# Kernel optimization log

Measured on AMD Instinct MI355X. Metric: run time of the kernel, lower is better.

## Reference

```python
import jax, jax.numpy as jnp
import numpy as np

H = 256        # hidden_dim == num_features
C = 10         # num_classes
N = 100000     # nodes
E = 1600000    # edges
BN_EPS = 1e-5
NEG_SLOPE = 0.1


def _bn(h, gamma, beta):
    # training-mode BatchNorm1d over node dim, biased variance (torch semantics)
    mu = jnp.mean(h, axis=0)
    var = jnp.mean(jnp.square(h - mu), axis=0)
    return (h - mu) * jax.lax.rsqrt(var + BN_EPS) * gamma + beta


def setup_inputs() -> dict:
    key = jax.random.key(0)
    ks = jax.random.split(key, 12)
    s = 1.0 / np.sqrt(H)
    x = jax.random.normal(ks[0], (N, H), dtype=jnp.float32)
    edge_index = jax.random.randint(ks[1], (2, E), 0, N, dtype=jnp.int64)
    return {
        "x": x,
        "edge_index": edge_index,
        # GIN MLP: lin1 -> bn -> relu -> lin2
        "W1": jax.random.uniform(ks[2], (H, H), jnp.float32, -s, s),
        "b1": jnp.zeros((H,), jnp.float32),
        "g_mlp": jnp.ones((H,), jnp.float32),
        "be_mlp": jnp.zeros((H,), jnp.float32),
        "W2": jax.random.uniform(ks[3], (H, H), jnp.float32, -s, s),
        "b2": jnp.zeros((H,), jnp.float32),
        # bn4
        "g4": jnp.ones((H,), jnp.float32),
        "be4": jnp.zeros((H,), jnp.float32),
        # head
        "Wl1": jax.random.uniform(ks[4], (H, H // 2), jnp.float32, -s, s),
        "bl1": jnp.zeros((H // 2,), jnp.float32),
        "Wl3": jax.random.uniform(ks[5], (H // 2, C), jnp.float32, -s, s),
        "bl3": jnp.zeros((C,), jnp.float32),
    }


def reference(x, edge_index, W1, b1, g_mlp, be_mlp, W2, b2, g4, be4, Wl1, bl1, Wl3, bl3):
    lrelu = lambda h: jax.nn.leaky_relu(h, NEG_SLOPE)
    src, dst = edge_index[0], edge_index[1]
    # GINConv: sum-aggregate neighbor messages (source_to_target), eps=0
    agg = jax.ops.segment_sum(x[src], dst, num_segments=x.shape[0])  # [N,H]
    h = agg + x  # (1+eps)*x + sum
    # PyG MLP([H,H,H]): lin -> batch_norm -> relu -> lin (plain last)
    h = jax.nn.relu(_bn(h @ W1 + b1, g_mlp, be_mlp)) @ W2 + b2
    x1 = lrelu(h)                     # relu(conv1(...), 0.1); dropout p=0
    h = lrelu(x1)                     # relu(x1, 0.1)
    h = lrelu(_bn(h, g4, be4))        # relu(bn4(x), 0.1); dropout p=0
    h = x + 0.01 * h                  # residual with original features
    h = lrelu(h @ Wl1 + bl1)
    return h @ Wl3 + bl3              # [N, C]
```

## Files before the change

### kernel.cpp

```cpp
#include <hip/hip_runtime.h>

constexpr int NN = 100000;
constexpr int NE = 1600000;
constexpr int HD = 256;
constexpr int NBUCK = 782;
constexpr int CGRID = 98;

typedef __attribute__((ext_vector_type(4))) float  f32x4;
typedef __attribute__((ext_vector_type(2))) float  f32x2;
typedef __attribute__((ext_vector_type(8))) short  bf16x8;

#if defined(__has_builtin)
#if __has_builtin(__builtin_amdgcn_cvt_pk_f32_fp8) && __has_builtin(__builtin_amdgcn_cvt_pk_fp8_f32)
#define HAVE_FP8_CVT 1
#endif
#endif
#ifndef HAVE_FP8_CVT
#define HAVE_FP8_CVT 0
#endif

__device__ __forceinline__ float bf2f(unsigned short u) {
  union { unsigned int i; float f; } c;
  c.i = ((unsigned int)u) << 16;
  return c.f;
}
__device__ __forceinline__ short f2bf(float f) {
  union { float f; unsigned int i; } c; c.f = f;
  unsigned int i = c.i + 0x7fffu + ((c.i >> 16) & 1u);
  return (short)(i >> 16);
}

__device__ __forceinline__ void gload16(const void* g, void* l) {
  __builtin_amdgcn_global_load_lds(
      (const __attribute__((address_space(1))) unsigned int*)g,
      (__attribute__((address_space(3))) unsigned int*)l, 16, 0, 0);
}

__global__ void k_detect(const int* __restrict__ ew, int* __restrict__ flag) {
  __shared__ int bad;
  if (threadIdx.x == 0) bad = 0;
  __syncthreads();
  int nz = 0;
  for (int i = threadIdx.x; i < 2048; i += 256) nz |= ew[2 * i + 1];
  if (nz) atomicOr(&bad, 1);
  __syncthreads();
  if (threadIdx.x == 0) *flag = (bad == 0) ? 1 : 0;
}

__global__ void k_cvtW(const float* __restrict__ W1, const float* __restrict__ W2,
                       const float* __restrict__ Wl1, const float* __restrict__ Wl3,
                       short* __restrict__ W1T, short* __restrict__ W2T,
                       short* __restrict__ Wl1T, short* __restrict__ Wl3T) {
  int b = blockIdx.x, t = threadIdx.x;
  if (b < 256)       W1T[b * 256 + t]        = f2bf(W1[t * 256 + b]);
  else if (b < 512){ int n = b - 256; W2T[n * 256 + t]  = f2bf(W2[t * 256 + n]); }
  else if (b < 640){ int n = b - 512; Wl1T[n * 256 + t] = f2bf(Wl1[t * 128 + n]); }
  else {
    if (t < 128) {
#pragma unroll
      for (int c = 0; c < 16; ++c)
        Wl3T[c * 128 + t] = (c < 10) ? f2bf(Wl3[t * 10 + c]) : (short)0;
    }
  }
}

#if HAVE_FP8_CVT
__global__ void k_cvtX(const float* __restrict__ x, void* __restrict__ xq) {
  int c = blockIdx.x * 256 + threadIdx.x;
  float4 a = ((const float4*)x)[2 * (size_t)c];
  float4 b = ((const float4*)x)[2 * (size_t)c + 1];
  int p0 = 0, p1 = 0;
  p0 = __builtin_amdgcn_cvt_pk_fp8_f32(a.x, a.y, p0, false);
  p0 = __builtin_amdgcn_cvt_pk_fp8_f32(a.z, a.w, p0, true);
  p1 = __builtin_amdgcn_cvt_pk_fp8_f32(b.x, b.y, p1, false);
  p1 = __builtin_amdgcn_cvt_pk_fp8_f32(b.z, b.w, p1, true);
  ((int2*)xq)[c] = make_int2(p0, p1);
}
#else
__global__ void k_cvtX(const float* __restrict__ x, void* __restrict__ xq) {
  int c = blockIdx.x * 256 + threadIdx.x;
  float4 a = ((const float4*)x)[2 * (size_t)c];
  float4 b = ((const float4*)x)[2 * (size_t)c + 1];
  bf16x8 o;
  o[0] = f2bf(a.x); o[1] = f2bf(a.y); o[2] = f2bf(a.z); o[3] = f2bf(a.w);
  o[4] = f2bf(b.x); o[5] = f2bf(b.y); o[6] = f2bf(b.z); o[7] = f2bf(b.w);
  ((bf16x8*)xq)[c] = o;
}
#endif

__global__ __launch_bounds__(1024) void k_count(const int* __restrict__ ew,
                                                const int* __restrict__ flag,
                                                int* __restrict__ cntmat) {
  __shared__ int lcnt[NBUCK];
  int m64 = *flag;
  int t = threadIdx.x;
  for (int i = t; i < NBUCK; i += 1024) lcnt[i] = 0;
  __syncthreads();
  int base = blockIdx.x * 16384;
#pragma unroll
  for (int u = 0; u < 16; u++) {
    int e = base + u * 1024 + t;
    if (e < NE) {
      int d = m64 ? ew[2 * (NE + e)] : ew[NE + e];
      atomicAdd(&lcnt[d >> 7], 1);
    }
  }
  __syncthreads();
  for (int i = t; i < NBUCK; i += 1024) cntmat[blockIdx.x * NBUCK + i] = lcnt[i];
}

__global__ __launch_bounds__(1024) void k_colscan(int* __restrict__ cntmat,
                                                  int* __restrict__ bases,
                                                  int* __restrict__ off_) {
  __shared__ int tot[1024];
  int t = threadIdx.x;
  int sum = 0;
  if (t < NBUCK) {
    for (int g = 0; g < CGRID; g++) sum += cntmat[g * NBUCK + t];
    tot[t] = sum;
  }
  __syncthreads();
  int v = (t < NBUCK) ? sum : 0;
  for (int o = 1; o < 1024; o <<= 1) {
    int u = (t >= o && t < NBUCK) ? tot[t - o] : 0;
    __syncthreads();
    if (t < NBUCK) tot[t] += u;
    __syncthreads();
  }
  if (t < NBUCK) {
    int b = tot[t] - v;
    bases[t] = b;
    int run = b;
    for (int g = 0; g < CGRID; g++) {
      int c = cntmat[g * NBUCK + t];
      cntmat[g * NBUCK + t] = run;
      run += c;
    }
  }
  if (t == NBUCK) bases[NBUCK] = NE;
  if (t == NBUCK + 1) off_[NN] = NE;
}

__global__ __launch_bounds__(1024) void k_scatter(const int* __restrict__ ew,
                                                  const int* __restrict__ flag,
                                                  const int* __restrict__ cntmat,
                                                  int* __restrict__ pairs) {
  __shared__ int lcur[NBUCK];
  int m64 = *flag;
  int t = threadIdx.x;
  for (int i = t; i < NBUCK; i += 1024) lcur[i] = cntmat[blockIdx.x * NBUCK + i];
  __syncthreads();
  int base = blockIdx.x * 16384;
#pragma unroll
  for (int u = 0; u < 16; u++) {
    int e = base + u * 1024 + t;
    if (e < NE) {
      int d = m64 ? ew[2 * (NE + e)] : ew[NE + e];
      int s = m64 ? ew[2 * e] : ew[e];
      int slot = atomicAdd(&lcur[d >> 7], 1);
      pairs[slot] = s | ((d & 127) << 17);
    }
  }
}

__global__ __launch_bounds__(256) void k_bsort(const int* __restrict__ pairs,
                                               const int* __restrict__ bases,
                                               int* __restrict__ off_,
                                               int* __restrict__ csr) {
  __shared__ int lcnt[128], lofs[128], lcur[128];
  int b = blockIdx.x, t = threadIdx.x;
  int s0 = bases[b], s1 = bases[b + 1];
  if (t < 128) lcnt[t] = 0;
  __syncthreads();
  for (int j = s0 + t; j < s1; j += 256) atomicAdd(&lcnt[(pairs[j] >> 17) & 127], 1);
  __syncthreads();
  int v = (t < 128) ? lcnt[t] : 0;
  if (t < 128) lofs[t] = v;
  __syncthreads();
  for (int o = 1; o < 128; o <<= 1) {
    int u = (t >= o && t < 128) ? lofs[t - o] : 0;
    __syncthreads();
    if (t < 128) lofs[t] += u;
    __syncthreads();
  }
  if (t < 128) {
    int ex = lofs[t] - v;
    lcur[t] = ex;
    int node = b * 128 + t;
    if (node < NN) off_[node] = s0 + ex;
  }
  __syncthreads();
  for (int j = s0 + t; j < s1; j += 256) {
    int p = pairs[j];
    int slot = atomicAdd(&lcur[(p >> 17) & 127], 1);
    csr[s0 + slot] = p & 0x1FFFF;
  }
}

#if HAVE_FP8_CVT
__global__ __launch_bounds__(256) void k_agg2(const void* __restrict__ xq,
                                              const int* __restrict__ off_,
                                              const int* __restrict__ csr,
                                              short* __restrict__ h0) {
  int node = blockIdx.x * 4 + (threadIdx.x >> 6);
  int lane = threadIdx.x & 63;
  const unsigned char* xb = (const unsigned char*)xq;
  size_t boff = (size_t)lane * 4;
  int s0 = off_[node], s1 = off_[node + 1];
  int sw = *(const int*)(xb + (size_t)node * 256 + boff);
  f32x2 slo = __builtin_amdgcn_cvt_pk_f32_fp8(sw, false);
  f32x2 shi = __builtin_amdgcn_cvt_pk_f32_fp8(sw, true);
  float a0 = slo[0], a1 = slo[1], a2 = shi[0], a3 = shi[1];
  int j = s0;
  while (j + 8 <= s1) {
    int idx[8];
#pragma unroll
    for (int u = 0; u < 8; u++) idx[u] = csr[j + u];
    int w[8];
#pragma unroll
    for (int u = 0; u < 8; u++) w[u] = *(const int*)(xb + (size_t)idx[u] * 256 + boff);
#pragma unroll
    for (int u = 0; u < 8; u++) {
      f32x2 lo = __builtin_amdgcn_cvt_pk_f32_fp8(w[u], false);
      f32x2 hi = __builtin_amdgcn_cvt_pk_f32_fp8(w[u], true);
      a0 += lo[0]; a1 += lo[1]; a2 += hi[0]; a3 += hi[1];
    }
    j += 8;
  }
  if (j + 4 <= s1) {
    int idx[4];
#pragma unroll
    for (int u = 0; u < 4; u++) idx[u] = csr[j + u];
    int w[4];
#pragma unroll
    for (int u = 0; u < 4; u++) w[u] = *(const int*)(xb + (size_t)idx[u] * 256 + boff);
#pragma unroll
    for (int u = 0; u < 4; u++) {
      f32x2 lo = __builtin_amdgcn_cvt_pk_f32_fp8(w[u], false);
      f32x2 hi = __builtin_amdgcn_cvt_pk_f32_fp8(w[u], true);
      a0 += lo[0]; a1 += lo[1]; a2 += hi[0]; a3 += hi[1];
    }
    j += 4;
  }
  for (; j < s1; j++) {
    int s = csr[j];
    int w = *(const int*)(xb + (size_t)s * 256 + boff);
    f32x2 lo = __builtin_amdgcn_cvt_pk_f32_fp8(w, false);
    f32x2 hi = __builtin_amdgcn_cvt_pk_f32_fp8(w, true);
    a0 += lo[0]; a1 += lo[1]; a2 += hi[0]; a3 += hi[1];
  }
  ushort4 o;
  o.x = (ushort)f2bf(a0); o.y = (ushort)f2bf(a1);
  o.z = (ushort)f2bf(a2); o.w = (ushort)f2bf(a3);
  *(ushort4*)((ushort*)h0 + (size_t)node * 256 + (size_t)lane * 4) = o;
}
#else
__global__ __launch_bounds__(256) void k_agg2(const void* __restrict__ xq,
                                              const int* __restrict__ off_,
                                              const int* __restrict__ csr,
                                              short* __restrict__ h0) {
  int node = blockIdx.x * 4 + (threadIdx.x >> 6);
  int lane = threadIdx.x & 63;
  const ushort* xu = (const ushort*)xq;
  size_t coff = (size_t)lane * 4;
  int s0 = off_[node], s1 = off_[node + 1];
  ushort4 sv = *(const ushort4*)(xu + (size_t)node * 256 + coff);
  float a0 = bf2f(sv.x), a1 = bf2f(sv.y), a2 = bf2f(sv.z), a3 = bf2f(sv.w);
  int j = s0;
  while (j + 8 <= s1) {
    int idx[8];
#pragma unroll
    for (int u = 0; u < 8; u++) idx[u] = csr[j + u];
    ushort4 v[8];
#pragma unroll
    for (int u = 0; u < 8; u++) v[u] = *(const ushort4*)(xu + (size_t)idx[u] * 256 + coff);
#pragma unroll
    for (int u = 0; u < 8; u++) {
      a0 += bf2f(v[u].x); a1 += bf2f(v[u].y);
      a2 += bf2f(v[u].z); a3 += bf2f(v[u].w);
    }
    j += 8;
  }
  for (; j < s1; j++) {
    int s = csr[j];
    ushort4 v = *(const ushort4*)(xu + (size_t)s * 256 + coff);
    a0 += bf2f(v.x); a1 += bf2f(v.y); a2 += bf2f(v.z); a3 += bf2f(v.w);
  }
  ushort4 o;
  o.x = (ushort)f2bf(a0); o.y = (ushort)f2bf(a1);
  o.z = (ushort)f2bf(a2); o.w = (ushort)f2bf(a3);
  *(ushort4*)((ushort*)h0 + (size_t)node * 256 + coff) = o;
}
#endif

template <int ACT, int TIN, int STATS>
__global__ __launch_bounds__(256, 2) void k_gemm(const short* __restrict__ A,
                                              const short* __restrict__ BT,
                                              const float* __restrict__ bias,
                                              short* __restrict__ C, int M,
                                              const float* __restrict__ tsc,
                                              const float* __restrict__ tsh,
                                              float* __restrict__ gsum,
                                              float* __restrict__ gssq) {
  __shared__ char smem[65536];
  __shared__ float lsc[256], lsh[256];
  __shared__ float lsum[128], lssq[128];
  int tid = threadIdx.x;
  int lane = tid & 63, w = tid >> 6;
  if (TIN) { lsc[tid] = tsc[tid]; lsh[tid] = tsh[tid]; }
  if (STATS && tid < 128) { lsum[tid] = 0.f; lssq[tid] = 0.f; }
  int bm = blockIdx.x >> 1, bn = blockIdx.x & 1;
  int bm0 = bm * 128, bn0 = bn * 128;
  int wm = w >> 1, wn = w & 1;
  int lr = lane & 15, lg = lane >> 4;
  f32x4 acc[4][4] = {};
  __syncthreads();

  bf16x8 stg[4];

#pragma unroll 1
  for (int it = 0; it < 4; ++it) {
    int b = it & 1;
    if (it == 0) {
      if (TIN) {
#pragma unroll
        for (int i = 0; i < 4; ++i) {
          int p = tid + 256 * i, row = p >> 3, s = (p & 7) ^ (row & 7);
          int grow = bm0 + row; if (grow > M - 1) grow = M - 1;
          stg[i] = *(const bf16x8*)(A + (size_t)grow * 256 + s * 8);
        }
      } else {
#pragma unroll
        for (int q = 0; q < 4; ++q) {
          int wc = w * 4 + q;
          int p = wc * 64 + lane, row = p >> 3, s = (p & 7) ^ (row & 7);
          int grow = bm0 + row; if (grow > M - 1) grow = M - 1;
          gload16(A + (size_t)grow * 256 + s * 8, smem + wc * 1024);
        }
      }
#pragma unroll
      for (int q = 0; q < 4; ++q) {
        int wc = w * 4 + q;
        int p = wc * 64 + lane, row = p >> 3, s = (p & 7) ^ (row & 7);
        gload16(BT + (size_t)(bn0 + row) * 256 + s * 8, smem + 16384 + wc * 1024);
      }
      if (TIN) {
#pragma unroll
        for (int i = 0; i < 4; ++i) {
          int p = tid + 256 * i, row = p >> 3, s = (p & 7) ^ (row & 7);
          int k0 = s * 8;
          float4 sc0 = *(const float4*)&lsc[k0], sc1 = *(const float4*)&lsc[k0 + 4];
          float4 sh0 = *(const float4*)&lsh[k0], sh1 = *(const float4*)&lsh[k0 + 4];
          bf16x8 v = stg[i], o;
          o[0] = f2bf(fmaxf(bf2f((unsigned short)v[0]) * sc0.x + sh0.x, 0.f));
          o[1] = f2bf(fmaxf(bf2f((unsigned short)v[1]) * sc0.y + sh0.y, 0.f));
          o[2] = f2bf(fmaxf(bf2f((unsigned short)v[2]) * sc0.z + sh0.z, 0.f));
          o[3] = f2bf(fmaxf(bf2f((unsigned short)v[3]) * sc0.w + sh0.w, 0.f));
          o[4] = f2bf(fmaxf(bf2f((unsigned short)v[4]) * sc1.x + sh1.x, 0.f));
          o[5] = f2bf(fmaxf(bf2f((unsigned short)v[5]) * sc1.y + sh1.y, 0.f));
          o[6] = f2bf(fmaxf(bf2f((unsigned short)v[6]) * sc1.z + sh1.z, 0.f));
          o[7] = f2bf(fmaxf(bf2f((unsigned short)v[7]) * sc1.w + sh1.w, 0.f));
          *(bf16x8*)(smem + p * 16) = o;
        }
      }
      __syncthreads();
    }
    int ktn = (it + 1) * 64;
    if (it < 3) {
      char* nb = smem + (b ^ 1) * 32768;
      if (TIN) {
#pragma unroll
        for (int i = 0; i < 4; ++i) {
          int p = tid + 256 * i, row = p >> 3, s = (p & 7) ^ (row & 7);
          int grow = bm0 + row; if (grow > M - 1) grow = M - 1;
          stg[i] = *(const bf16x8*)(A + (size_t)grow * 256 + ktn + s * 8);
        }
      } else {
#pragma unroll
        for (int q = 0; q < 4; ++q) {
          int wc = w * 4 + q;
          int p = wc * 64 + lane, row = p >> 3, s = (p & 7) ^ (row & 7);
          int grow = bm0 + row; if (grow > M - 1) grow = M - 1;
          gload16(A + (size_t)grow * 256 + ktn + s * 8, nb + wc * 1024);
        }
      }
#pragma unroll
      for (int q = 0; q < 4; ++q) {
        int wc = w * 4 + q;
        int p = wc * 64 + lane, row = p >> 3, s = (p & 7) ^ (row & 7);
        gload16(BT + (size_t)(bn0 + row) * 256 + ktn + s * 8, nb + 16384 + wc * 1024);
      }
    }
    const char* sa = smem + b * 32768;
    const char* sb = sa + 16384;
#pragma unroll
    for (int ks = 0; ks < 2; ++ks) {
      bf16x8 af[4], bfr[4];
#pragma unroll
      for (int mi = 0; mi < 4; ++mi) {
        int row = wm * 64 + mi * 16 + lr;
        int q = (lg + 4 * ks) ^ (row & 7);
        af[mi] = *(const bf16x8*)(sa + row * 128 + q * 16);
      }
#pragma unroll
      for (int ni = 0; ni < 4; ++ni) {
        int row = wn * 64 + ni * 16 + lr;
        int q = (lg + 4 * ks) ^ (row & 7);
        bfr[ni] = *(const bf16x8*)(sb + row * 128 + q * 16);
      }
#pragma unroll
      for (int mi = 0; mi < 4; ++mi)
#pragma unroll
        for (int ni = 0; ni < 4; ++ni)
          acc[mi][ni] = __builtin_amdgcn_mfma_f32_16x16x32_bf16(af[mi], bfr[ni], acc[mi][ni], 0, 0, 0);
    }
    if (TIN && it < 3) {
      char* nb = smem + (b ^ 1) * 32768;
#pragma unroll
      for (int i = 0; i < 4; ++i) {
        int p = tid + 256 * i, row = p >> 3, s = (p & 7) ^ (row & 7);
        int k0 = ktn + s * 8;
        float4 sc0 = *(const float4*)&lsc[k0], sc1 = *(const float4*)&lsc[k0 + 4];
        float4 sh0 = *(const float4*)&lsh[k0], sh1 = *(const float4*)&lsh[k0 + 4];
        bf16x8 v = stg[i], o;
        o[0] = f2bf(fmaxf(bf2f((unsigned short)v[0]) * sc0.x + sh0.x, 0.f));
        o[1] = f2bf(fmaxf(bf2f((unsigned short)v[1]) * sc0.y + sh0.y, 0.f));
        o[2] = f2bf(fmaxf(bf2f((unsigned short)v[2]) * sc0.z + sh0.z, 0.f));
        o[3] = f2bf(fmaxf(bf2f((unsigned short)v[3]) * sc0.w + sh0.w, 0.f));
        o[4] = f2bf(fmaxf(bf2f((unsigned short)v[4]) * sc1.x + sh1.x, 0.f));
        o[5] = f2bf(fmaxf(bf2f((unsigned short)v[5]) * sc1.y + sh1.y, 0.f));
        o[6] = f2bf(fmaxf(bf2f((unsigned short)v[6]) * sc1.z + sh1.z, 0.f));
        o[7] = f2bf(fmaxf(bf2f((unsigned short)v[7]) * sc1.w + sh1.w, 0.f));
        *(bf16x8*)(nb + p * 16) = o;
      }
    }
    __syncthreads();
  }

  short* zs = (short*)smem;
#pragma unroll
  for (int ni = 0; ni < 4; ++ni) {
    int col = wn * 64 + ni * 16 + lr;
    float bv = bias[bn0 + col];
    float ps = 0.f, pq = 0.f;
#pragma unroll
    for (int mi = 0; mi < 4; ++mi) {
#pragma unroll
      for (int r = 0; r < 4; ++r) {
        int row = wm * 64 + mi * 16 + lg * 4 + r;
        float tv = acc[mi][ni][r] + bv;
        if (ACT == 1) tv = tv > 0.f ? tv : 0.01f * tv;
        if (STATS && (bm0 + row) < M) { ps += tv; pq += tv * tv; }
        zs[row * 136 + col] = f2bf(tv);
      }
    }
    if (STATS) {
      ps += __shfl_xor(ps, 16); pq += __shfl_xor(pq, 16);
      ps += __shfl_xor(ps, 32); pq += __shfl_xor(pq, 32);
      if (lane < 16) {
        atomicAdd(&lsum[wn * 64 + ni * 16 + lane], ps);
        atomicAdd(&lssq[wn * 64 + ni * 16 + lane], pq);
      }
    }
  }
  __syncthreads();
  {
    int row = tid >> 1;
    int grow = bm0 + row;
    if (grow < M) {
#pragma unroll
      for (int i = 0; i < 8; ++i) {
        int cs = (tid & 1) * 8 + i;
        bf16x8 v = *(const bf16x8*)((const char*)zs + row * 272 + cs * 16);
        *(bf16x8*)(C + (size_t)grow * 256 + bn0 + cs * 8) = v;
      }
    }
  }
  if (STATS) {
    if (tid < 128) {
      atomicAdd(&gsum[bn0 + tid], lsum[tid]);
      atomicAdd(&gssq[bn0 + tid], lssq[tid]);
    }
  }
}

__global__ void k_bnprep(const float* __restrict__ sum, const float* __restrict__ ssq,
                         const float* __restrict__ g, const float* __restrict__ be,
                         float* __restrict__ scale, float* __restrict__ shift, int M) {
  int c = threadIdx.x;
  float mu = sum[c] / (float)M;
  float var = ssq[c] / (float)M - mu * mu;
  float rs = rsqrtf(var + 1e-5f);
  float sc = g[c] * rs;
  scale[c] = sc;
  shift[c] = be[c] - mu * sc;
}

__global__ __launch_bounds__(256, 2) void k_head(const short* __restrict__ V,
                                                 const float* __restrict__ x,
                                                 const short* __restrict__ BT,
                                                 const float* __restrict__ bl1,
                                                 const short* __restrict__ wl3t,
                                                 const float* __restrict__ bl3,
                                                 const float* __restrict__ tsc,
                                                 const float* __restrict__ tsh,
                                                 float* __restrict__ out, int M) {
  __shared__ char smem[65536];
  __shared__ float lsc[256], lsh[256];
  __shared__ short wl3s[2048];
  int tid = threadIdx.x;
  int lane = tid & 63, w = tid >> 6;
  lsc[tid] = tsc[tid]; lsh[tid] = tsh[tid];
  {
    int p = w * 64 + lane;
    gload16(wl3t + (size_t)p * 8, (char*)wl3s + w * 1024);
  }
  int bm0 = blockIdx.x * 128;
  int wm = w >> 1, wn = w & 1;
  int lr = lane & 15, lg = lane >> 4;
  f32x4 acc[4][4] = {};
  __syncthreads();

  bf16x8 stgv[4];
  float stgx[4][8];

#pragma unroll 1
  for (int it = 0; it < 4; ++it) {
    int b = it & 1;
    if (it == 0) {
#pragma unroll
      for (int i = 0; i < 4; ++i) {
        int p = tid + 256 * i, row = p >> 3, s = (p & 7) ^ (row & 7);
        int grow = bm0 + row; if (grow > M - 1) grow = M - 1;
        size_t base = (size_t)grow * 256 + s * 8;
        stgv[i] = *(const bf16x8*)(V + base);
        *(float4*)&stgx[i][0] = *(const float4*)(x + base);
        *(float4*)&stgx[i][4] = *(const float4*)(x + base + 4);
      }
#pragma unroll
      for (int q = 0; q < 4; ++q) {
        int wc = w * 4 + q;
        int p = wc * 64 + lane, row = p >> 3, s = (p & 7) ^ (row & 7);
        gload16(BT + (size_t)row * 256 + s * 8, smem + 16384 + wc * 1024);
      }
#pragma unroll
      for (int i = 0; i < 4; ++i) {
        int p = tid + 256 * i, row = p >> 3, s = (p & 7) ^ (row & 7);
        int k0 = s * 8;
        bf16x8 v = stgv[i], o;
#pragma unroll
        for (int jj = 0; jj < 8; ++jj) {
          float f = bf2f((unsigned short)v[jj]) * lsc[k0 + jj] + lsh[k0 + jj];
          f = f > 0.f ? f : 0.1f * f;
          o[jj] = f2bf(stgx[i][jj] + 0.01f * f);
        }
        *(bf16x8*)(smem + p * 16) = o;
      }
      __syncthreads();
    }
    int ktn = (it + 1) * 64;
    if (it < 3) {
      char* nb = smem + (b ^ 1) * 32768;
#pragma unroll
      for (int i = 0; i < 4; ++i) {
        int p = tid + 256 * i, row = p >> 3, s = (p & 7) ^ (row & 7);
        int grow = bm0 + row; if (grow > M - 1) grow = M - 1;
        size_t base = (size_t)grow * 256 + ktn + s * 8;
        stgv[i] = *(const bf16x8*)(V + base);
        *(float4*)&stgx[i][0] = *(const float4*)(x + base);
        *(float4*)&stgx[i][4] = *(const float4*)(x + base + 4);
      }
#pragma unroll
      for (int q = 0; q < 4; ++q) {
        int wc = w * 4 + q;
        int p = wc * 64 + lane, row = p >> 3, s = (p & 7) ^ (row & 7);
        gload16(BT + (size_t)row * 256 + ktn + s * 8, nb + 16384 + wc * 1024);
      }
    }
    const char* sa = smem + b * 32768;
    const char* sb = sa + 16384;
#pragma unroll
    for (int ks = 0; ks < 2; ++ks) {
      bf16x8 af[4], bfr[4];
#pragma unroll
      for (int mi = 0; mi < 4; ++mi) {
        int row = wm * 64 + mi * 16 + lr;
        int q = (lg + 4 * ks) ^ (row & 7);
        af[mi] = *(const bf16x8*)(sa + row * 128 + q * 16);
      }
#pragma unroll
      for (int ni = 0; ni < 4; ++ni) {
        int row = wn * 64 + ni * 16 + lr;
        int q = (lg + 4 * ks) ^ (row & 7);
        bfr[ni] = *(const bf16x8*)(sb + row * 128 + q * 16);
      }
#pragma unroll
      for (int mi = 0; mi < 4; ++mi)
#pragma unroll
        for (int ni = 0; ni < 4; ++ni)
          acc[mi][ni] = __builtin_amdgcn_mfma_f32_16x16x32_bf16(af[mi], bfr[ni], acc[mi][ni], 0, 0, 0);
    }
    if (it < 3) {
      char* nb = smem + (b ^ 1) * 32768;
#pragma unroll
      for (int i = 0; i < 4; ++i) {
        int p = tid + 256 * i, row = p >> 3, s = (p & 7) ^ (row & 7);
        int k0 = ktn + s * 8;
        bf16x8 v = stgv[i], o;
#pragma unroll
        for (int jj = 0; jj < 8; ++jj) {
          float f = bf2f((unsigned short)v[jj]) * lsc[k0 + jj] + lsh[k0 + jj];
          f = f > 0.f ? f : 0.1f * f;
          o[jj] = f2bf(stgx[i][jj] + 0.01f * f);
        }
        *(bf16x8*)(nb + p * 16) = o;
      }
    }
    __syncthreads();
  }

  short* zs = (short*)smem;
#pragma unroll
  for (int ni = 0; ni < 4; ++ni) {
    int col = wn * 64 + ni * 16 + lr;
    float bv = bl1[col];
#pragma unroll
    for (int mi = 0; mi < 4; ++mi) {
#pragma unroll
      for (int r = 0; r < 4; ++r) {
        int row = wm * 64 + mi * 16 + lg * 4 + r;
        float tv = acc[mi][ni][r] + bv;
        tv = tv > 0.f ? tv : 0.1f * tv;
        zs[row * 136 + col] = f2bf(tv);
      }
    }
  }
  __syncthreads();

  f32x4 acc2[2] = {};
#pragma unroll
  for (int kk = 0; kk < 4; ++kk) {
    bf16x8 bfr = *(const bf16x8*)((const char*)wl3s + lr * 256 + (kk * 4 + lg) * 16);
#pragma unroll
    for (int m = 0; m < 2; ++m) {
      int row = (w * 2 + m) * 16 + lr;
      bf16x8 af = *(const bf16x8*)((const char*)zs + row * 272 + (kk * 4 + lg) * 16);
      acc2[m] = __builtin_amdgcn_mfma_f32_16x16x32_bf16(af, bfr, acc2[m], 0, 0, 0);
    }
  }
  if (lr < 10) {
    float bv = bl3[lr];
#pragma unroll
    for (int m = 0; m < 2; ++m) {
#pragma unroll
      for (int r = 0; r < 4; ++r) {
        int row = (w * 2 + m) * 16 + lg * 4 + r;
        int grow = bm0 + row;
        if (grow < M) out[(size_t)grow * 10 + lr] = acc2[m][r] + bv;
      }
    }
  }
}

extern "C" void kernel_launch(void* const* d_in, const int* in_sizes, int n_in,
                              void* d_out, int out_size, void* d_ws, size_t ws_size,
                              hipStream_t stream) {
  const float* x   = (const float*)d_in[0];
  const int*   ew  = (const int*)d_in[1];
  const float* W1  = (const float*)d_in[2];
  const float* b1  = (const float*)d_in[3];
  const float* g1  = (const float*)d_in[4];
  const float* be1 = (const float*)d_in[5];
  const float* W2  = (const float*)d_in[6];
  const float* b2  = (const float*)d_in[7];
  const float* g4  = (const float*)d_in[8];
  const float* be4 = (const float*)d_in[9];
  const float* Wl1 = (const float*)d_in[10];
  const float* bl1 = (const float*)d_in[11];
  const float* Wl3 = (const float*)d_in[12];
  const float* bl3 = (const float*)d_in[13];
  float* out = (float*)d_out;

  char* ws = (char*)d_ws;
  const size_t OFF_OFF  = 0;
  const size_t OFF_BASES= 400128;
  const size_t OFF_CNT  = 800256;
  const size_t OFF_WL3T = 1106944;
  const size_t OFF_STATS= 1200384;
  const size_t OFF_BN   = 1204480;
  const size_t OFF_FLAG = 1208576;
  const size_t OFF_W1T  = 1209216;
  const size_t OFF_W2T  = 1340288;
  const size_t OFF_WL1T = 1471360;
  const size_t OFF_CSR  = 1536896;
  const size_t OFF_BUFA = 7936896;
  const size_t OFF_BUFB = 59136896;
  if (ws_size < 110336896) return;

  int* off_  = (int*)(ws + OFF_OFF);
  int* bases_= (int*)(ws + OFF_BASES);
  int* cnt_  = (int*)(ws + OFF_CNT);
  float* sum1 = (float*)(ws + OFF_STATS);
  float* ssq1 = sum1 + 256;
  float* sum4 = sum1 + 512;
  float* ssq4 = sum1 + 768;
  float* sc1 = (float*)(ws + OFF_BN);
  float* sh1 = sc1 + 256;
  float* sc4 = sc1 + 512;
  float* sh4 = sc1 + 768;
  int* flag_ = (int*)(ws + OFF_FLAG);
  short* W1T  = (short*)(ws + OFF_W1T);
  short* W2T  = (short*)(ws + OFF_W2T);
  short* Wl1T = (short*)(ws + OFF_WL1T);
  short* Wl3T = (short*)(ws + OFF_WL3T);
  int* csr_   = (int*)(ws + OFF_CSR);
  short* bufA = (short*)(ws + OFF_BUFA);
  short* bufB = (short*)(ws + OFF_BUFB);
  int* pairs_ = (int*)(ws + OFF_BUFA);
  void* xq    = (void*)bufB;

  hipMemsetAsync(ws + OFF_STATS, 0, 4096, stream);
  k_detect<<<1, 256, 0, stream>>>(ew, flag_);
  k_cvtW<<<641, 256, 0, stream>>>(W1, W2, Wl1, Wl3, W1T, W2T, Wl1T, Wl3T);
  k_cvtX<<<12500, 256, 0, stream>>>(x, xq);
  k_count<<<CGRID, 1024, 0, stream>>>(ew, flag_, cnt_);
  k_colscan<<<1, 1024, 0, stream>>>(cnt_, bases_, off_);
  k_scatter<<<CGRID, 1024, 0, stream>>>(ew, flag_, cnt_, pairs_);
  k_bsort<<<NBUCK, 256, 0, stream>>>(pairs_, bases_, off_, csr_);
  k_agg2<<<25000, 256, 0, stream>>>(xq, off_, csr_, bufA);
  k_gemm<0, 0, 1><<<1564, 256, 0, stream>>>(bufA, W1T, b1, bufB, NN,
                                            nullptr, nullptr, sum1, ssq1);
  k_bnprep<<<1, 256, 0, stream>>>(sum1, ssq1, g1, be1, sc1, sh1, NN);
  k_gemm<1, 1, 1><<<1564, 256, 0, stream>>>(bufB, W2T, b2, bufA, NN,
                                            sc1, sh1, sum4, ssq4);
  k_bnprep<<<1, 256, 0, stream>>>(sum4, ssq4, g4, be4, sc4, sh4, NN);
  k_head<<<782, 256, 0, stream>>>(bufA, x, Wl1T, bl1, Wl3T, bl3, sc4, sh4, out, NN);
}
```

Before: 300.4 us.

## Switch MLP GEMMs and intermediate activations from bf16 to fp8

Stores the aggregated features, both MLP GEMM outputs and the W1/W2 weights in fp8 instead of bf16, and replaces the bf16 MFMA with the fp8 16x16x32 MFMA. The LDS layout is reworked so two rows share a 128-byte swizzled unit, and shared memory per GEMM block is halved. This roughly halves memory traffic for the intermediate activations and GEMM operands, at the cost of much lower precision on pre-BatchNorm activations. The stats-buffer memset is also folded into the detect kernel to save a launch.

```diff
diff --git a/kernel.cpp b/kernel.cpp
--- a/kernel.cpp
+++ b/kernel.cpp
@@ -2,22 +2,12 @@
 
 constexpr int NN = 100000;
 constexpr int NE = 1600000;
-constexpr int HD = 256;
 constexpr int NBUCK = 782;
 constexpr int CGRID = 98;
 
 typedef __attribute__((ext_vector_type(4))) float  f32x4;
 typedef __attribute__((ext_vector_type(2))) float  f32x2;
 typedef __attribute__((ext_vector_type(8))) short  bf16x8;
-
-#if defined(__has_builtin)
-#if __has_builtin(__builtin_amdgcn_cvt_pk_f32_fp8) && __has_builtin(__builtin_amdgcn_cvt_pk_fp8_f32)
-#define HAVE_FP8_CVT 1
-#endif
-#endif
-#ifndef HAVE_FP8_CVT
-#define HAVE_FP8_CVT 0
-#endif
 
 __device__ __forceinline__ float bf2f(unsigned short u) {
   union { unsigned int i; float f; } c;
@@ -29,6 +19,15 @@
   unsigned int i = c.i + 0x7fffu + ((c.i >> 16) & 1u);
   return (short)(i >> 16);
 }
+__device__ __forceinline__ unsigned char f2fp8(float f) {
+  int w = __builtin_amdgcn_cvt_pk_fp8_f32(f, 0.f, 0, false);
+  return (unsigned char)(w & 0xff);
+}
+__device__ __forceinline__ void up4(int wv, float* f) {
+  f32x2 a = __builtin_amdgcn_cvt_pk_f32_fp8(wv, false);
+  f32x2 b = __builtin_amdgcn_cvt_pk_f32_fp8(wv, true);
+  f[0] = a[0]; f[1] = a[1]; f[2] = b[0]; f[3] = b[1];
+}
 
 __device__ __forceinline__ void gload16(const void* g, void* l) {
   __builtin_amdgcn_global_load_lds(
@@ -36,9 +35,11 @@
       (__attribute__((address_space(3))) unsigned int*)l, 16, 0, 0);
 }
 
-__global__ void k_detect(const int* __restrict__ ew, int* __restrict__ flag) {
+__global__ void k_detect(const int* __restrict__ ew, int* __restrict__ flag,
+                         float* __restrict__ zst) {
   __shared__ int bad;
   if (threadIdx.x == 0) bad = 0;
+  for (int i = threadIdx.x; i < 1024; i += 256) zst[i] = 0.f;
   __syncthreads();
   int nz = 0;
   for (int i = threadIdx.x; i < 2048; i += 256) nz |= ew[2 * i + 1];
@@ -49,11 +50,11 @@
 
 __global__ void k_cvtW(const float* __restrict__ W1, const float* __restrict__ W2,
                        const float* __restrict__ Wl1, const float* __restrict__ Wl3,
-                       short* __restrict__ W1T, short* __restrict__ W2T,
+                       unsigned char* __restrict__ W1T8, unsigned char* __restrict__ W2T8,
                        short* __restrict__ Wl1T, short* __restrict__ Wl3T) {
   int b = blockIdx.x, t = threadIdx.x;
-  if (b < 256)       W1T[b * 256 + t]        = f2bf(W1[t * 256 + b]);
-  else if (b < 512){ int n = b - 256; W2T[n * 256 + t]  = f2bf(W2[t * 256 + n]); }
+  if (b < 256)       W1T8[b * 256 + t]       = f2fp8(W1[t * 256 + b]);
+  else if (b < 512){ int n = b - 256; W2T8[n * 256 + t] = f2fp8(W2[t * 256 + n]); }
   else if (b < 640){ int n = b - 512; Wl1T[n * 256 + t] = f2bf(Wl1[t * 128 + n]); }
   else {
     if (t < 128) {
@@ -64,7 +65,6 @@
   }
 }
 
-#if HAVE_FP8_CVT
 __global__ void k_cvtX(const float* __restrict__ x, void* __restrict__ xq) {
   int c = blockIdx.x * 256 + threadIdx.x;
   float4 a = ((const float4*)x)[2 * (size_t)c];
@@ -76,17 +76,6 @@
   p1 = __builtin_amdgcn_cvt_pk_fp8_f32(b.z, b.w, p1, true);
   ((int2*)xq)[c] = make_int2(p0, p1);
 }
-#else
-__global__ void k_cvtX(const float* __restrict__ x, void* __restrict__ xq) {
-  int c = blockIdx.x * 256 + threadIdx.x;
-  float4 a = ((const float4*)x)[2 * (size_t)c];
-  float4 b = ((const float4*)x)[2 * (size_t)c + 1];
-  bf16x8 o;
-  o[0] = f2bf(a.x); o[1] = f2bf(a.y); o[2] = f2bf(a.z); o[3] = f2bf(a.w);
-  o[4] = f2bf(b.x); o[5] = f2bf(b.y); o[6] = f2bf(b.z); o[7] = f2bf(b.w);
-  ((bf16x8*)xq)[c] = o;
-}
-#endif
 
 __global__ __launch_bounds__(1024) void k_count(const int* __restrict__ ew,
                                                 const int* __restrict__ flag,
@@ -197,11 +186,10 @@
   }
 }
 
-#if HAVE_FP8_CVT
 __global__ __launch_bounds__(256) void k_agg2(const void* __restrict__ xq,
                                               const int* __restrict__ off_,
                                               const int* __restrict__ csr,
-                                              short* __restrict__ h0) {
+                                              unsigned char* __restrict__ h0) {
   int node = blockIdx.x * 4 + (threadIdx.x >> 6);
   int lane = threadIdx.x & 63;
   const unsigned char* xb = (const unsigned char*)xq;
@@ -249,64 +237,22 @@
     f32x2 hi = __builtin_amdgcn_cvt_pk_f32_fp8(w, true);
     a0 += lo[0]; a1 += lo[1]; a2 += hi[0]; a3 += hi[1];
   }
-  ushort4 o;
-  o.x = (ushort)f2bf(a0); o.y = (ushort)f2bf(a1);
-  o.z = (ushort)f2bf(a2); o.w = (ushort)f2bf(a3);
-  *(ushort4*)((ushort*)h0 + (size_t)node * 256 + (size_t)lane * 4) = o;
-}
-#else
-__global__ __launch_bounds__(256) void k_agg2(const void* __restrict__ xq,
-                                              const int* __restrict__ off_,
-                                              const int* __restrict__ csr,
-                                              short* __restrict__ h0) {
-  int node = blockIdx.x * 4 + (threadIdx.x >> 6);
-  int lane = threadIdx.x & 63;
-  const ushort* xu = (const ushort*)xq;
-  size_t coff = (size_t)lane * 4;
-  int s0 = off_[node], s1 = off_[node + 1];
-  ushort4 sv = *(const ushort4*)(xu + (size_t)node * 256 + coff);
-  float a0 = bf2f(sv.x), a1 = bf2f(sv.y), a2 = bf2f(sv.z), a3 = bf2f(sv.w);
-  int j = s0;
-  while (j + 8 <= s1) {
-    int idx[8];
-#pragma unroll
-    for (int u = 0; u < 8; u++) idx[u] = csr[j + u];
-    ushort4 v[8];
-#pragma unroll
-    for (int u = 0; u < 8; u++) v[u] = *(const ushort4*)(xu + (size_t)idx[u] * 256 + coff);
-#pragma unroll
-    for (int u = 0; u < 8; u++) {
-      a0 += bf2f(v[u].x); a1 += bf2f(v[u].y);
-      a2 += bf2f(v[u].z); a3 += bf2f(v[u].w);
-    }
-    j += 8;
-  }
-  for (; j < s1; j++) {
-    int s = csr[j];
-    ushort4 v = *(const ushort4*)(xu + (size_t)s * 256 + coff);
-    a0 += bf2f(v.x); a1 += bf2f(v.y); a2 += bf2f(v.z); a3 += bf2f(v.w);
-  }
-  ushort4 o;
-  o.x = (ushort)f2bf(a0); o.y = (ushort)f2bf(a1);
-  o.z = (ushort)f2bf(a2); o.w = (ushort)f2bf(a3);
-  *(ushort4*)((ushort*)h0 + (size_t)node * 256 + coff) = o;
-}
-#endif
+  int o = 0;
+  o = __builtin_amdgcn_cvt_pk_fp8_f32(a0, a1, o, false);
+  o = __builtin_amdgcn_cvt_pk_fp8_f32(a2, a3, o, true);
+  ((int*)h0)[(size_t)node * 64 + lane] = o;
+}
 
 template <int ACT, int TIN, int STATS>
-__global__ __launch_bounds__(256, 2) void k_gemm(const short* __restrict__ A,
-                                              const short* __restrict__ BT,
-                                              const float* __restrict__ bias,
-                                              short* __restrict__ C, int M,
-                                              const float* __restrict__ tsc,
-                                              const float* __restrict__ tsh,
-                                              float* __restrict__ gsum,
-                                              float* __restrict__ gssq) {
-  __shared__ char smem[65536];
+__global__ __launch_bounds__(256, 2) void k_gemm8(
+    const unsigned char* __restrict__ A, const unsigned char* __restrict__ BT,
+    const float* __restrict__ bias, unsigned char* __restrict__ C, int M,
+    const float* __restrict__ tsc, const float* __restrict__ tsh,
+    float* __restrict__ gsum, float* __restrict__ gssq) {
+  __shared__ char smem[32768];
   __shared__ float lsc[256], lsh[256];
   __shared__ float lsum[128], lssq[128];
-  int tid = threadIdx.x;
-  int lane = tid & 63, w = tid >> 6;
+  int tid = threadIdx.x, lane = tid & 63, w = tid >> 6;
   if (TIN) { lsc[tid] = tsc[tid]; lsh[tid] = tsh[tid]; }
   if (STATS && tid < 128) { lsum[tid] = 0.f; lssq[tid] = 0.f; }
   int bm = blockIdx.x >> 1, bn = blockIdx.x & 1;
@@ -316,7 +262,7 @@
   f32x4 acc[4][4] = {};
   __syncthreads();
 
-  bf16x8 stg[4];
+  int4 stg[2];
 
 #pragma unroll 1
   for (int it = 0; it < 4; ++it) {
@@ -324,120 +270,136 @@
     if (it == 0) {
       if (TIN) {
 #pragma unroll
-        for (int i = 0; i < 4; ++i) {
-          int p = tid + 256 * i, row = p >> 3, s = (p & 7) ^ (row & 7);
-          int grow = bm0 + row; if (grow > M - 1) grow = M - 1;
-          stg[i] = *(const bf16x8*)(A + (size_t)grow * 256 + s * 8);
+        for (int i = 0; i < 2; ++i) {
+          int p = i * 256 + tid, unit = p >> 3, u = (p & 7) ^ (unit & 7);
+          int srow = unit * 2 + (u >> 2), slot = u & 3;
+          int grow = bm0 + srow; if (grow > M - 1) grow = M - 1;
+          stg[i] = *(const int4*)(A + (size_t)grow * 256 + slot * 16);
         }
       } else {
 #pragma unroll
-        for (int q = 0; q < 4; ++q) {
-          int wc = w * 4 + q;
-          int p = wc * 64 + lane, row = p >> 3, s = (p & 7) ^ (row & 7);
-          int grow = bm0 + row; if (grow > M - 1) grow = M - 1;
-          gload16(A + (size_t)grow * 256 + s * 8, smem + wc * 1024);
+        for (int q = 0; q < 2; ++q) {
+          int wc = w * 2 + q;
+          int p = wc * 64 + lane, unit = p >> 3, u = (p & 7) ^ (unit & 7);
+          int srow = unit * 2 + (u >> 2), slot = u & 3;
+          int grow = bm0 + srow; if (grow > M - 1) grow = M - 1;
+          gload16(A + (size_t)grow * 256 + slot * 16, smem + wc * 1024);
         }
       }
 #pragma unroll
-      for (int q = 0; q < 4; ++q) {
-        int wc = w * 4 + q;
-        int p = wc * 64 + lane, row = p >> 3, s = (p & 7) ^ (row & 7);
-        gload16(BT + (size_t)(bn0 + row) * 256 + s * 8, smem + 16384 + wc * 1024);
+      for (int q = 0; q < 2; ++q) {
+        int wc = w * 2 + q;
+        int p = wc * 64 + lane, unit = p >> 3, u = (p & 7) ^ (unit & 7);
+        int srow = unit * 2 + (u >> 2), slot = u & 3;
+        gload16(BT + (size_t)(bn0 + srow) * 256 + slot * 16, smem + 8192 + wc * 1024);
       }
       if (TIN) {
 #pragma unroll
-        for (int i = 0; i < 4; ++i) {
-          int p = tid + 256 * i, row = p >> 3, s = (p & 7) ^ (row & 7);
-          int k0 = s * 8;
-          float4 sc0 = *(const float4*)&lsc[k0], sc1 = *(const float4*)&lsc[k0 + 4];
-          float4 sh0 = *(const float4*)&lsh[k0], sh1 = *(const float4*)&lsh[k0 + 4];
-          bf16x8 v = stg[i], o;
-          o[0] = f2bf(fmaxf(bf2f((unsigned short)v[0]) * sc0.x + sh0.x, 0.f));
-          o[1] = f2bf(fmaxf(bf2f((unsigned short)v[1]) * sc0.y + sh0.y, 0.f));
-          o[2] = f2bf(fmaxf(bf2f((unsigned short)v[2]) * sc0.z + sh0.z, 0.f));
-          o[3] = f2bf(fmaxf(bf2f((unsigned short)v[3]) * sc0.w + sh0.w, 0.f));
-          o[4] = f2bf(fmaxf(bf2f((unsigned short)v[4]) * sc1.x + sh1.x, 0.f));
-          o[5] = f2bf(fmaxf(bf2f((unsigned short)v[5]) * sc1.y + sh1.y, 0.f));
-          o[6] = f2bf(fmaxf(bf2f((unsigned short)v[6]) * sc1.z + sh1.z, 0.f));
-          o[7] = f2bf(fmaxf(bf2f((unsigned short)v[7]) * sc1.w + sh1.w, 0.f));
-          *(bf16x8*)(smem + p * 16) = o;
+        for (int i = 0; i < 2; ++i) {
+          int p = i * 256 + tid, unit = p >> 3, u = (p & 7) ^ (unit & 7);
+          int slot = u & 3;
+          int k0 = slot * 16;
+          float f[16];
+          up4(stg[i].x, f); up4(stg[i].y, f + 4); up4(stg[i].z, f + 8); up4(stg[i].w, f + 12);
+#pragma unroll
+          for (int jj = 0; jj < 16; ++jj) f[jj] = fmaxf(f[jj] * lsc[k0 + jj] + lsh[k0 + jj], 0.f);
+          int w0 = 0, w1 = 0, w2 = 0, w3 = 0;
+          w0 = __builtin_amdgcn_cvt_pk_fp8_f32(f[0], f[1], w0, false);
+          w0 = __builtin_amdgcn_cvt_pk_fp8_f32(f[2], f[3], w0, true);
+          w1 = __builtin_amdgcn_cvt_pk_fp8_f32(f[4], f[5], w1, false);
+          w1 = __builtin_amdgcn_cvt_pk_fp8_f32(f[6], f[7], w1, true);
+          w2 = __builtin_amdgcn_cvt_pk_fp8_f32(f[8], f[9], w2, false);
+          w2 = __builtin_amdgcn_cvt_pk_fp8_f32(f[10], f[11], w2, true);
+          w3 = __builtin_amdgcn_cvt_pk_fp8_f32(f[12], f[13], w3, false);
+          w3 = __builtin_amdgcn_cvt_pk_fp8_f32(f[14], f[15], w3, true);
+          *(int4*)(smem + p * 16) = make_int4(w0, w1, w2, w3);
         }
       }
       __syncthreads();
     }
     int ktn = (it + 1) * 64;
     if (it < 3) {
-      char* nb = smem + (b ^ 1) * 32768;
+      char* nb = smem + (b ^ 1) * 16384;
       if (TIN) {
 #pragma unroll
-        for (int i = 0; i < 4; ++i) {
-          int p = tid + 256 * i, row = p >> 3, s = (p & 7) ^ (row & 7);
-          int grow = bm0 + row; if (grow > M - 1) grow = M - 1;
-          stg[i] = *(const bf16x8*)(A + (size_t)grow * 256 + ktn + s * 8);
+        for (int i = 0; i < 2; ++i) {
+          int p = i * 256 + tid, unit = p >> 3, u = (p & 7) ^ (unit & 7);
+          int srow = unit * 2 + (u >> 2), slot = u & 3;
+          int grow = bm0 + srow; if (grow > M - 1) grow = M - 1;
+          stg[i] = *(const int4*)(A + (size_t)grow * 256 + ktn + slot * 16);
         }
       } else {
 #pragma unroll
-        for (int q = 0; q < 4; ++q) {
-          int wc = w * 4 + q;
-          int p = wc * 64 + lane, row = p >> 3, s = (p & 7) ^ (row & 7);
-          int grow = bm0 + row; if (grow > M - 1) grow = M - 1;
-          gload16(A + (size_t)grow * 256 + ktn + s * 8, nb + wc * 1024);
+        for (int q = 0; q < 2; ++q) {
+          int wc = w * 2 + q;
+          int p = wc * 64 + lane, unit = p >> 3, u = (p & 7) ^ (unit & 7);
+          int srow = unit * 2 + (u >> 2), slot = u & 3;
+          int grow = bm0 + srow; if (grow > M - 1) grow = M - 1;
+          gload16(A + (size_t)grow * 256 + ktn + slot * 16, nb + wc * 1024);
         }
       }
 #pragma unroll
-      for (int q = 0; q < 4; ++q) {
-        int wc = w * 4 + q;
-        int p = wc * 64 + lane, row = p >> 3, s = (p & 7) ^ (row & 7);
-        gload16(BT + (size_t)(bn0 + row) * 256 + ktn + s * 8, nb + 16384 + wc * 1024);
-      }
-    }
-    const char* sa = smem + b * 32768;
-    const char* sb = sa + 16384;
+      for (int q = 0; q < 2; ++q) {
+        int wc = w * 2 + q;
+        int p = wc * 64 + lane, unit = p >> 3, u = (p & 7) ^ (unit & 7);
+        int srow = unit * 2 + (u >> 2), slot = u & 3;
+        gload16(BT + (size_t)(bn0 + srow) * 256 + ktn + slot * 16, nb + 8192 + wc * 1024);
+      }
+    }
+    const char* sa = smem + b * 16384;
+    const char* sb = sa + 8192;
 #pragma unroll
     for (int ks = 0; ks < 2; ++ks) {
-      bf16x8 af[4], bfr[4];
+      long af[4], bfr[4];
 #pragma unroll
       for (int mi = 0; mi < 4; ++mi) {
         int row = wm * 64 + mi * 16 + lr;
-        int q = (lg + 4 * ks) ^ (row & 7);
-        af[mi] = *(const bf16x8*)(sa + row * 128 + q * 16);
+        int unit = row >> 1;
+        int u = (row & 1) * 4 + ks * 2 + (lg >> 1);
+        int up = u ^ (unit & 7);
+        af[mi] = *(const long*)(sa + unit * 128 + up * 16 + (lg & 1) * 8);
       }
 #pragma unroll
       for (int ni = 0; ni < 4; ++ni) {
         int row = wn * 64 + ni * 16 + lr;
-        int q = (lg + 4 * ks) ^ (row & 7);
-        bfr[ni] = *(const bf16x8*)(sb + row * 128 + q * 16);
+        int unit = row >> 1;
+        int u = (row & 1) * 4 + ks * 2 + (lg >> 1);
+        int up = u ^ (unit & 7);
+        bfr[ni] = *(const long*)(sb + unit * 128 + up * 16 + (lg & 1) * 8);
       }
 #pragma unroll
       for (int mi = 0; mi < 4; ++mi)
 #pragma unroll
         for (int ni = 0; ni < 4; ++ni)
-          acc[mi][ni] = __builtin_amdgcn_mfma_f32_16x16x32_bf16(af[mi], bfr[ni], acc[mi][ni], 0, 0, 0);
+          acc[mi][ni] = __builtin_amdgcn_mfma_f32_16x16x32_fp8_fp8(af[mi], bfr[ni], acc[mi][ni], 0, 0, 0);
     }
     if (TIN && it < 3) {
-      char* nb = smem + (b ^ 1) * 32768;
-#pragma unroll
-      for (int i = 0; i < 4; ++i) {
-        int p = tid + 256 * i, row = p >> 3, s = (p & 7) ^ (row & 7);
-        int k0 = ktn + s * 8;
-        float4 sc0 = *(const float4*)&lsc[k0], sc1 = *(const float4*)&lsc[k0 + 4];
-        float4 sh0 = *(const float4*)&lsh[k0], sh1 = *(const float4*)&lsh[k0 + 4];
-        bf16x8 v = stg[i], o;
-        o[0] = f2bf(fmaxf(bf2f((unsigned short)v[0]) * sc0.x + sh0.x, 0.f));
-        o[1] = f2bf(fmaxf(bf2f((unsigned short)v[1]) * sc0.y + sh0.y, 0.f));
-        o[2] = f2bf(fmaxf(bf2f((unsigned short)v[2]) * sc0.z + sh0.z, 0.f));
-        o[3] = f2bf(fmaxf(bf2f((unsigned short)v[3]) * sc0.w + sh0.w, 0.f));
-        o[4] = f2bf(fmaxf(bf2f((unsigned short)v[4]) * sc1.x + sh1.x, 0.f));
-        o[5] = f2bf(fmaxf(bf2f((unsigned short)v[5]) * sc1.y + sh1.y, 0.f));
-        o[6] = f2bf(fmaxf(bf2f((unsigned short)v[6]) * sc1.z + sh1.z, 0.f));
-        o[7] = f2bf(fmaxf(bf2f((unsigned short)v[7]) * sc1.w + sh1.w, 0.f));
-        *(bf16x8*)(nb + p * 16) = o;
+      char* nb = smem + (b ^ 1) * 16384;
+#pragma unroll
+      for (int i = 0; i < 2; ++i) {
+        int p = i * 256 + tid, unit = p >> 3, u = (p & 7) ^ (unit & 7);
+        int slot = u & 3;
+        int k0 = ktn + slot * 16;
+        float f[16];
+        up4(stg[i].x, f); up4(stg[i].y, f + 4); up4(stg[i].z, f + 8); up4(stg[i].w, f + 12);
+#pragma unroll
+        for (int jj = 0; jj < 16; ++jj) f[jj] = fmaxf(f[jj] * lsc[k0 + jj] + lsh[k0 + jj], 0.f);
+        int w0 = 0, w1 = 0, w2 = 0, w3 = 0;
+        w0 = __builtin_amdgcn_cvt_pk_fp8_f32(f[0], f[1], w0, false);
+        w0 = __builtin_amdgcn_cvt_pk_fp8_f32(f[2], f[3], w0, true);
+        w1 = __builtin_amdgcn_cvt_pk_fp8_f32(f[4], f[5], w1, false);
+        w1 = __builtin_amdgcn_cvt_pk_fp8_f32(f[6], f[7], w1, true);
+        w2 = __builtin_amdgcn_cvt_pk_fp8_f32(f[8], f[9], w2, false);
+        w2 = __builtin_amdgcn_cvt_pk_fp8_f32(f[10], f[11], w2, true);
+        w3 = __builtin_amdgcn_cvt_pk_fp8_f32(f[12], f[13], w3, false);
+        w3 = __builtin_amdgcn_cvt_pk_fp8_f32(f[14], f[15], w3, true);
+        *(int4*)(nb + p * 16) = make_int4(w0, w1, w2, w3);
       }
     }
     __syncthreads();
   }
 
-  short* zs = (short*)smem;
+  unsigned char* zs = (unsigned char*)smem;
 #pragma unroll
   for (int ni = 0; ni < 4; ++ni) {
     int col = wn * 64 + ni * 16 + lr;
@@ -451,7 +413,7 @@
         float tv = acc[mi][ni][r] + bv;
         if (ACT == 1) tv = tv > 0.f ? tv : 0.01f * tv;
         if (STATS && (bm0 + row) < M) { ps += tv; pq += tv * tv; }
-        zs[row * 136 + col] = f2bf(tv);
+        zs[row * 144 + col] = f2fp8(tv);
       }
     }
     if (STATS) {
@@ -469,10 +431,10 @@
     int grow = bm0 + row;
     if (grow < M) {
 #pragma unroll
-      for (int i = 0; i < 8; ++i) {
-        int cs = (tid & 1) * 8 + i;
-        bf16x8 v = *(const bf16x8*)((const char*)zs + row * 272 + cs * 16);
-        *(bf16x8*)(C + (size_t)grow * 256 + bn0 + cs * 8) = v;
+      for (int i = 0; i < 4; ++i) {
+        int cs = (tid & 1) * 64 + i * 16;
+        int4 v = *(const int4*)(zs + row * 144 + cs);
+        *(int4*)(C + (size_t)grow * 256 + bn0 + cs) = v;
       }
     }
   }
@@ -496,7 +458,7 @@
   shift[c] = be[c] - mu * sc;
 }
 
-__global__ __launch_bounds__(256, 2) void k_head(const short* __restrict__ V,
+__global__ __launch_bounds__(256, 2) void k_head(const unsigned char* __restrict__ Vq,
                                                  const float* __restrict__ x,
                                                  const short* __restrict__ BT,
                                                  const float* __restrict__ bl1,
@@ -521,7 +483,7 @@
   f32x4 acc[4][4] = {};
   __syncthreads();
 
-  bf16x8 stgv[4];
+  int2 stgv[4];
   float stgx[4][8];
 
 #pragma unroll 1
@@ -533,7 +495,7 @@
         int p = tid + 256 * i, row = p >> 3, s = (p & 7) ^ (row & 7);
         int grow = bm0 + row; if (grow > M - 1) grow = M - 1;
         size_t base = (size_t)grow * 256 + s * 8;
-        stgv[i] = *(const bf16x8*)(V + base);
+        stgv[i] = *(const int2*)(Vq + base);
         *(float4*)&stgx[i][0] = *(const float4*)(x + base);
         *(float4*)&stgx[i][4] = *(const float4*)(x + base + 4);
       }
@@ -547,10 +509,12 @@
       for (int i = 0; i < 4; ++i) {
         int p = tid + 256 * i, row = p >> 3, s = (p & 7) ^ (row & 7);
         int k0 = s * 8;
-        bf16x8 v = stgv[i], o;
+        float fv[8];
+        up4(stgv[i].x, fv); up4(stgv[i].y, fv + 4);
+        bf16x8 o;
 #pragma unroll
         for (int jj = 0; jj < 8; ++jj) {
-          float f = bf2f((unsigned short)v[jj]) * lsc[k0 + jj] + lsh[k0 + jj];
+          float f = fv[jj] * lsc[k0 + jj] + lsh[k0 + jj];
           f = f > 0.f ? f : 0.1f * f;
           o[jj] = f2bf(stgx[i][jj] + 0.01f * f);
         }
@@ -566,7 +530,7 @@
         int p = tid + 256 * i, row = p >> 3, s = (p & 7) ^ (row & 7);
         int grow = bm0 + row; if (grow > M - 1) grow = M - 1;
         size_t base = (size_t)grow * 256 + ktn + s * 8;
-        stgv[i] = *(const bf16x8*)(V + base);
+        stgv[i] = *(const int2*)(Vq + base);
         *(float4*)&stgx[i][0] = *(const float4*)(x + base);
         *(float4*)&stgx[i][4] = *(const float4*)(x + base + 4);
       }
@@ -606,10 +570,12 @@
       for (int i = 0; i < 4; ++i) {
         int p = tid + 256 * i, row = p >> 3, s = (p & 7) ^ (row & 7);
         int k0 = ktn + s * 8;
-        bf16x8 v = stgv[i], o;
+        float fv[8];
+        up4(stgv[i].x, fv); up4(stgv[i].y, fv + 4);
+        bf16x8 o;
 #pragma unroll
         for (int jj = 0; jj < 8; ++jj) {
-          float f = bf2f((unsigned short)v[jj]) * lsc[k0 + jj] + lsh[k0 + jj];
+          float f = fv[jj] * lsc[k0 + jj] + lsh[k0 + jj];
           f = f > 0.f ? f : 0.1f * f;
           o[jj] = f2bf(stgx[i][jj] + 0.01f * f);
         }
@@ -709,30 +675,29 @@
   float* sc4 = sc1 + 512;
   float* sh4 = sc1 + 768;
   int* flag_ = (int*)(ws + OFF_FLAG);
-  short* W1T  = (short*)(ws + OFF_W1T);
-  short* W2T  = (short*)(ws + OFF_W2T);
+  unsigned char* W1T8 = (unsigned char*)(ws + OFF_W1T);
+  unsigned char* W2T8 = (unsigned char*)(ws + OFF_W2T);
   short* Wl1T = (short*)(ws + OFF_WL1T);
   short* Wl3T = (short*)(ws + OFF_WL3T);
   int* csr_   = (int*)(ws + OFF_CSR);
-  short* bufA = (short*)(ws + OFF_BUFA);
-  short* bufB = (short*)(ws + OFF_BUFB);
+  unsigned char* bufA = (unsigned char*)(ws + OFF_BUFA);
+  unsigned char* bufB = (unsigned char*)(ws + OFF_BUFB);
   int* pairs_ = (int*)(ws + OFF_BUFA);
   void* xq    = (void*)bufB;
 
-  hipMemsetAsync(ws + OFF_STATS, 0, 4096, stream);
-  k_detect<<<1, 256, 0, stream>>>(ew, flag_);
-  k_cvtW<<<641, 256, 0, stream>>>(W1, W2, Wl1, Wl3, W1T, W2T, Wl1T, Wl3T);
+  k_detect<<<1, 256, 0, stream>>>(ew, flag_, sum1);
+  k_cvtW<<<641, 256, 0, stream>>>(W1, W2, Wl1, Wl3, W1T8, W2T8, Wl1T, Wl3T);
   k_cvtX<<<12500, 256, 0, stream>>>(x, xq);
   k_count<<<CGRID, 1024, 0, stream>>>(ew, flag_, cnt_);
   k_colscan<<<1, 1024, 0, stream>>>(cnt_, bases_, off_);
   k_scatter<<<CGRID, 1024, 0, stream>>>(ew, flag_, cnt_, pairs_);
   k_bsort<<<NBUCK, 256, 0, stream>>>(pairs_, bases_, off_, csr_);
   k_agg2<<<25000, 256, 0, stream>>>(xq, off_, csr_, bufA);
-  k_gemm<0, 0, 1><<<1564, 256, 0, stream>>>(bufA, W1T, b1, bufB, NN,
-                                            nullptr, nullptr, sum1, ssq1);
+  k_gemm8<0, 0, 1><<<1564, 256, 0, stream>>>(bufA, W1T8, b1, bufB, NN,
+                                             nullptr, nullptr, sum1, ssq1);
   k_bnprep<<<1, 256, 0, stream>>>(sum1, ssq1, g1, be1, sc1, sh1, NN);
-  k_gemm<1, 1, 1><<<1564, 256, 0, stream>>>(bufB, W2T, b2, bufA, NN,
-                                            sc1, sh1, sum4, ssq4);
+  k_gemm8<1, 1, 1><<<1564, 256, 0, stream>>>(bufB, W2T8, b2, bufA, NN,
+                                             sc1, sh1, sum4, ssq4);
   k_bnprep<<<1, 256, 0, stream>>>(sum4, ssq4, g4, be4, sc4, sh4, NN);
   k_head<<<782, 256, 0, stream>>>(bufA, x, Wl1T, bl1, Wl3T, bl3, sc4, sh4, out, NN);
 }
```

Measured after the change: 267.4 us. 1.12x faster.
